# Kernel tuning notes

Measured on AMD Instinct MI355X. Metric: run time of the kernel, lower is better.

The kernel has to match this reference:

```python
import jax, jax.numpy as jnp
import numpy as np

B, T, D, H = 4, 2048, 1024, 16
DK = D // H


def setup_inputs() -> dict:
    key = jax.random.key(0)
    ks = jax.random.split(key, 9)
    s = 1.0 / np.sqrt(D)
    x = jax.random.normal(ks[0], (B, T, D), dtype=jnp.float32)
    mask = jnp.tril(jnp.ones((T, T), dtype=bool))[None, None]  # causal [1,1,T,T]
    wq = jax.random.uniform(ks[1], (D, D), jnp.float32, -s, s)
    bq = jax.random.uniform(ks[2], (D,), jnp.float32, -s, s)
    wk = jax.random.uniform(ks[3], (D, D), jnp.float32, -s, s)
    bk = jax.random.uniform(ks[4], (D,), jnp.float32, -s, s)
    wv = jax.random.uniform(ks[5], (D, D), jnp.float32, -s, s)
    bv = jax.random.uniform(ks[6], (D,), jnp.float32, -s, s)
    wo = jax.random.uniform(ks[7], (D, D), jnp.float32, -s, s)
    bo = jax.random.uniform(ks[8], (D,), jnp.float32, -s, s)
    return {"x": x, "mask": mask, "wq": wq, "bq": bq, "wk": wk, "bk": bk,
            "wv": wv, "bv": bv, "wo": wo, "bo": bo}


def reference(x, mask, wq, bq, wk, bk, wv, bv, wo, bo):
    # projections: torch Linear is x @ W.T + b; here weights stored as (D, D) used directly
    q = (x @ wq + bq).reshape(B, T, H, DK).transpose(0, 2, 1, 3)  # [B,H,T,dk]
    k = (x @ wk + bk).reshape(B, T, H, DK).transpose(0, 2, 1, 3)
    v = (x @ wv + bv).reshape(B, T, H, DK).transpose(0, 2, 1, 3)
    scores = jnp.einsum('bhqd,bhkd->bhqk', q, k) / jnp.sqrt(jnp.float32(DK))
    scores = jnp.where(mask, scores, -jnp.inf)
    attn = jax.nn.softmax(scores, axis=-1)
    # dropout p=0.0 -> identity
    y = jnp.einsum('bhqk,bhkd->bhqd', attn, v)
    y = y.transpose(0, 2, 1, 3).reshape(B, T, D)
    return y @ wo + bo
```

## Files before the change

### kernel.cpp

```cpp
#include <hip/hip_runtime.h>


typedef short s16x8 __attribute__((ext_vector_type(8)));
typedef short s16x4 __attribute__((ext_vector_type(4)));
typedef float f32x4 __attribute__((ext_vector_type(4)));
typedef unsigned int u32x2 __attribute__((ext_vector_type(2)));
typedef unsigned short u16x4 __attribute__((ext_vector_type(4)));

static __device__ __forceinline__ float bf2f(unsigned short u) {
    return __uint_as_float(((unsigned int)u) << 16);
}
static __device__ __forceinline__ unsigned short f2bf(float f) {
    unsigned int x = __float_as_uint(f);
    unsigned int r = x + 0x7fffu + ((x >> 16) & 1u);
    return (unsigned short)(r >> 16);
}

static __device__ __forceinline__ void gload_lds16(const short* g, short* l) {
    __builtin_amdgcn_global_load_lds((__attribute__((address_space(1))) void*)g,
                                     (__attribute__((address_space(3))) void*)l, 16, 0, 0);
}

static __device__ __forceinline__ unsigned int cvt_pk_bf16(float a, float b) {
    unsigned int r;
    asm("v_cvt_pk_bf16_f32 %0, %1, %2" : "=v"(r) : "v"(a), "v"(b));
    return r;
}

static __device__ __forceinline__ float fexp2(float x) {
    float r;
    asm("v_exp_f32 %0, %1" : "=v"(r) : "v"(x));
    return r;
}

__global__ __launch_bounds__(64) void detect_dtype(const unsigned short* __restrict__ x,
                                                   int* __restrict__ flag) {
    int lane = threadIdx.x;
    int cnt = 0;
    for (int i = 0; i < 64; ++i) {
        float v = bf2f(x[lane * 64 + i]);
        if (!(fabsf(v) < 1e10f)) cnt++;
    }
    unsigned long long m = __ballot(cnt > 0);
    if (lane == 0) *flag = (m != 0ull) ? 1 : 0;
}

__global__ __launch_bounds__(256) void prep(const void* __restrict__ x,
                                            const void* __restrict__ b0, const void* __restrict__ b1,
                                            const void* __restrict__ b2, const void* __restrict__ b3,
                                            const void* __restrict__ w0, const void* __restrict__ w1,
                                            const void* __restrict__ w2, const void* __restrict__ w3,
                                            unsigned short* __restrict__ xb,
                                            unsigned short* __restrict__ bb,
                                            unsigned short* __restrict__ wT,
                                            const int* __restrict__ flag) {
    __shared__ unsigned short t[32][33];
    int bid = blockIdx.x, tid = threadIdx.x;
    int f = *flag;
    if (bid < 8192) {
        int i = bid * 256 + tid;
        u16x4 o;
        if (f) {
            float4 v = ((const float4*)x)[i];
            o[0] = f2bf(v.x); o[1] = f2bf(v.y); o[2] = f2bf(v.z); o[3] = f2bf(v.w);
        } else {
            o = ((const u16x4*)x)[i];
        }
        ((u16x4*)xb)[i] = o;
    } else if (bid < 8208) {
        int i = (bid - 8192) * 256 + tid;
        const void* src = (i < 1024) ? b0 : (i < 2048 ? b1 : (i < 3072 ? b2 : b3));
        int k = i & 1023;
        bb[i] = f ? f2bf(((const float*)src)[k]) : ((const unsigned short*)src)[k];
    } else {
        int tz = bid - 8208;
        int z = tz >> 10, tile = tz & 1023;
        const void* src = (z == 0) ? w0 : (z == 1 ? w1 : (z == 2 ? w2 : w3));
        unsigned short* dst = wT + (size_t)z * 1024 * 1024;
        int xx = tid & 31, yy = tid >> 5;
        int n0 = (tile & 31) * 32, k0 = (tile >> 5) * 32;
        for (int j = 0; j < 32; j += 8) {
            size_t idx = (size_t)(k0 + yy + j) * 1024 + n0 + xx;
            t[yy + j][xx] = f ? f2bf(((const float*)src)[idx]) : ((const unsigned short*)src)[idx];
        }
        __syncthreads();
        for (int j = 0; j < 32; j += 8) dst[(size_t)(n0 + yy + j) * 1024 + k0 + xx] = t[xx][yy + j];
    }
}

__global__ __launch_bounds__(256) void gemm_bf16(const short* __restrict__ A,
                                                 const short* __restrict__ Bt,
                                                 void* __restrict__ C,
                                                 short* __restrict__ vt,
                                                 const unsigned short* __restrict__ bq,
                                                 const unsigned short* __restrict__ bk,
                                                 const unsigned short* __restrict__ bv,
                                                 int K, int ldc,
                                                 const int* __restrict__ flag, int f32out,
                                                 int scale_q, int fuse_v) {
    __shared__ __align__(16) short As[2][128][64];
    __shared__ __align__(16) short Bs[2][128][64];
    int tid = threadIdx.x;
    int wid = tid >> 6, lane = tid & 63, quad = lane >> 4, l16 = lane & 15;
    int wm = wid & 1, wn = wid >> 1;
    int m0 = blockIdx.x * 128, n0 = blockIdx.y * 128;
    bool wf = f32out && (*flag != 0);

    int srow = lane >> 3;
    int schunk = (lane & 7) ^ srow;
    const short* Ag = A  + (size_t)(m0 + wid * 32 + srow) * K + schunk * 8;
    const short* Bg = Bt + (size_t)(n0 + wid * 32 + srow) * K + schunk * 8;

    f32x4 acc[4][4] = {};
    int nt = K >> 6;

#pragma unroll
    for (int c = 0; c < 4; ++c) {
        gload_lds16(Ag + c * 8 * K, &As[0][wid * 32 + c * 8][0]);
        gload_lds16(Bg + c * 8 * K, &Bs[0][wid * 32 + c * 8][0]);
    }
    __syncthreads();

    for (int t = 0; t < nt; ++t) {
        if (t + 1 < nt) {
            int bu = (t + 1) & 1;
            int kof = (t + 1) * 64;
#pragma unroll
            for (int c = 0; c < 4; ++c) {
                gload_lds16(Ag + kof + c * 8 * K, &As[bu][wid * 32 + c * 8][0]);
                gload_lds16(Bg + kof + c * 8 * K, &Bs[bu][wid * 32 + c * 8][0]);
            }
        }
        const short (*Ab)[64] = As[t & 1];
#pragma unroll
        for (int kk = 0; kk < 2; ++kk) {
            s16x8 a[4], b[4];
#pragma unroll
            for (int i = 0; i < 4; ++i) {
                int row = wm * 64 + i * 16 + l16;
                a[i] = *(const s16x8*)&Ab[row][(((kk << 2) + quad) ^ (row & 7)) << 3];
            }
#pragma unroll
            for (int j = 0; j < 4; ++j) {
                int row = wn * 64 + j * 16 + l16;
                b[j] = *(const s16x8*)&Bs[t & 1][row][(((kk << 2) + quad) ^ (row & 7)) << 3];
            }
            __builtin_amdgcn_s_setprio(1);
#pragma unroll
            for (int i = 0; i < 4; ++i)
#pragma unroll
                for (int j = 0; j < 4; ++j)
                    acc[i][j] = __builtin_amdgcn_mfma_f32_16x16x32_bf16(a[i], b[j], acc[i][j], 0, 0, 0);
            __builtin_amdgcn_s_setprio(0);
        }
        __syncthreads();
    }
    for (int j = 0; j < 4; ++j) {
        int col = n0 + wn * 64 + j * 16 + l16;
        const unsigned short* bptr = (col < 1024) ? bq : (col < 2048 ? bk : bv);
        float bias = bf2f(bptr[col & 1023]);
        float cs = (scale_q && col < 1024) ? 0.18033688f : 1.0f;
        for (int i = 0; i < 4; ++i) {
            int rbase = m0 + wm * 64 + i * 16 + quad * 4;
            if (fuse_v && col >= 2048) {
                int h = (col - 2048) >> 6, dk = col & 63;
                int bb_ = rbase >> 11, t = rbase & 2047;
                s16x4 pk;
                for (int r = 0; r < 4; ++r) pk[r] = (short)f2bf(acc[i][j][r] + bias);
                *(s16x4*)(vt + ((size_t)((bb_ * 16 + h) * 64 + dk)) * 2048 + t) = pk;
            } else {
                for (int r = 0; r < 4; ++r) {
                    float v = (acc[i][j][r] + bias) * cs;
                    size_t idx = (size_t)(rbase + r) * ldc + col;
                    if (wf) ((float*)C)[idx] = v;
                    else    ((unsigned short*)C)[idx] = f2bf(v);
                }
            }
        }
    }
}

static __device__ __forceinline__ void stage_tiles(const short* kbase, const short* vbase,
                                                   int kt, short* Kb, short* Vb,
                                                   int wid, int lane) {
    int row = wid * 8 + (lane >> 3);
    int c_src = (lane & 7) ^ (lane >> 3);
    const short* kg = kbase + (size_t)(kt * 64 + row) * 3072 + c_src * 8;
    const short* vg = vbase + (size_t)row * 2048 + kt * 64 + c_src * 8;
    gload_lds16(kg, Kb + wid * 512);
    gload_lds16(vg, Vb + wid * 512);
}

static __device__ __forceinline__ s16x8 lds_frag(const short* buf, int row, int cg) {
    int slot = cg ^ (row & 7);
    return *(const s16x8*)(buf + row * 64 + slot * 8);
}

__global__ __launch_bounds__(512, 4) void attn(const short* __restrict__ qkv,
                                               const short* __restrict__ vt,
                                               unsigned short* __restrict__ y) {
    __shared__ __align__(16) short Kbuf[3][64 * 64];
    __shared__ __align__(16) short Vbuf[3][64 * 64];
    __shared__ __align__(16) short Ps[8][16 * 68];
    int tid = threadIdx.x;
    int wid = tid >> 6, lane = tid & 63, quad = lane >> 4, l16 = lane & 15;
    int bh = blockIdx.x, b = bh >> 4, h = bh & 15;
    const short* kbase = qkv + (size_t)b * 2048 * 3072 + 1024 + h * 64;
    const short* vbase = vt + (size_t)bh * 64 * 2048;
    short* PsW = &Ps[wid][0];

    s16x8 ones;
    for (int e = 0; e < 8; ++e) ones[e] = (short)0x3F80;

    int qb = 15 - (int)blockIdx.y;
    int ktmax = 2 * qb + 1;
    int kmax_w = 2 * qb + (wid >> 2);

    const short* qp = qkv + (size_t)(b * 2048 + qb * 128 + wid * 16 + l16) * 3072 + h * 64;
    s16x8 q0 = *(const s16x8*)(qp + quad * 8);
    s16x8 q1 = *(const s16x8*)(qp + 32 + quad * 8);

    float m_old = -INFINITY;
    f32x4 lacc = {0.f, 0.f, 0.f, 0.f};
    f32x4 o[4] = {};
    s16x8 paA, paB;
    s16x8 vr[8];
    bool have_prev = false;

    stage_tiles(kbase, vbase, 0, &Kbuf[0][0], &Vbuf[0][0], wid, lane);
    stage_tiles(kbase, vbase, 1, &Kbuf[1][0], &Vbuf[1][0], wid, lane);
    int ss = 2;
    int cc = 0;

    for (int kt = 0; kt <= ktmax; ++kt) {
        if (kt < ktmax) asm volatile("s_waitcnt vmcnt(2)" ::: "memory");
        else            asm volatile("s_waitcnt vmcnt(0)" ::: "memory");
        __builtin_amdgcn_sched_barrier(0);
        __builtin_amdgcn_s_barrier();

        if (kt + 2 <= ktmax) {
            stage_tiles(kbase, vbase, kt + 2, &Kbuf[0][0] + ss * 4096, &Vbuf[0][0] + ss * 4096,
                        wid, lane);
            ss = (ss == 2) ? 0 : ss + 1;
        }

        if (kt <= kmax_w) {
            const short* Kb = &Kbuf[0][0] + cc * 4096;
            const short* Vb = &Vbuf[0][0] + cc * 4096;

            f32x4 s[4] = {};
            __builtin_amdgcn_s_setprio(1);
            for (int j = 0; j < 4; ++j) {
                s16x8 klo = lds_frag(Kb, j * 16 + l16, quad);
                s16x8 khi = lds_frag(Kb, j * 16 + l16, 4 + quad);
                s[j] = __builtin_amdgcn_mfma_f32_16x16x32_bf16(klo, q0, s[j], 0, 0, 0);
                s[j] = __builtin_amdgcn_mfma_f32_16x16x32_bf16(khi, q1, s[j], 0, 0, 0);
            }
            if (have_prev) {
                lacc = __builtin_amdgcn_mfma_f32_16x16x32_bf16(paA, ones, lacc, 0, 0, 0);
                lacc = __builtin_amdgcn_mfma_f32_16x16x32_bf16(paB, ones, lacc, 0, 0, 0);
                for (int d = 0; d < 4; ++d) {
                    o[d] = __builtin_amdgcn_mfma_f32_16x16x32_bf16(paA, vr[2 * d], o[d], 0, 0, 0);
                    o[d] = __builtin_amdgcn_mfma_f32_16x16x32_bf16(paB, vr[2 * d + 1], o[d], 0, 0, 0);
                }
            }
            __builtin_amdgcn_s_setprio(0);

            if (kt == kmax_w) {
                int qq = (wid & 3) * 16 + l16;
                for (int j = 0; j < 4; ++j)
                    for (int r = 0; r < 4; ++r)
                        if (j * 16 + quad * 4 + r > qq) s[j][r] = -INFINITY;
            }

            float mj0 = fmaxf(fmaxf(s[0][0], s[0][1]), s[0][2]);
            mj0 = fmaxf(mj0, s[0][3]);
            float mj1 = fmaxf(fmaxf(s[1][0], s[1][1]), s[1][2]);
            mj1 = fmaxf(mj1, s[1][3]);
            float mj2 = fmaxf(fmaxf(s[2][0], s[2][1]), s[2][2]);
            mj2 = fmaxf(mj2, s[2][3]);
            float mj3 = fmaxf(fmaxf(s[3][0], s[3][1]), s[3][2]);
            mj3 = fmaxf(mj3, s[3][3]);
            float mx = fmaxf(fmaxf(fmaxf(mj0, mj1), mj2), mj3);
            mx = fmaxf(mx, __shfl_xor(mx, 16));
            mx = fmaxf(mx, __shfl_xor(mx, 32));

            if (__any(mx > m_old + 8.0f)) {
                float mn = fmaxf(m_old, mx);
                float alpha = fexp2(m_old - mn);
                m_old = mn;
                float ar[4];
                for (int r = 0; r < 4; ++r) ar[r] = __shfl(alpha, quad * 4 + r);
                for (int r = 0; r < 4; ++r) {
                    lacc[r] *= ar[r];
                    for (int d = 0; d < 4; ++d) o[d][r] *= ar[r];
                }
            }

            for (int j = 0; j < 4; ++j) {
                float p0 = fexp2(s[j][0] - m_old);
                float p1 = fexp2(s[j][1] - m_old);
                float p2 = fexp2(s[j][2] - m_old);
                float p3 = fexp2(s[j][3] - m_old);
                u32x2 w;
                w.x = cvt_pk_bf16(p0, p1);
                w.y = cvt_pk_bf16(p2, p3);
                *(u32x2*)(PsW + l16 * 68 + j * 16 + quad * 4) = w;
            }
            paA = *(const s16x8*)&PsW[l16 * 68 + quad * 8];
            paB = *(const s16x8*)&PsW[l16 * 68 + 32 + quad * 8];

            for (int d = 0; d < 4; ++d) {
                vr[2 * d]     = lds_frag(Vb, d * 16 + l16, quad);
                vr[2 * d + 1] = lds_frag(Vb, d * 16 + l16, 4 + quad);
            }
            have_prev = true;
        }
        cc = (cc == 2) ? 0 : cc + 1;
    }

    if (have_prev) {
        __builtin_amdgcn_s_setprio(1);
        lacc = __builtin_amdgcn_mfma_f32_16x16x32_bf16(paA, ones, lacc, 0, 0, 0);
        lacc = __builtin_amdgcn_mfma_f32_16x16x32_bf16(paB, ones, lacc, 0, 0, 0);
        for (int d = 0; d < 4; ++d) {
            o[d] = __builtin_amdgcn_mfma_f32_16x16x32_bf16(paA, vr[2 * d], o[d], 0, 0, 0);
            o[d] = __builtin_amdgcn_mfma_f32_16x16x32_bf16(paB, vr[2 * d + 1], o[d], 0, 0, 0);
        }
        __builtin_amdgcn_s_setprio(0);
    }

    for (int r = 0; r < 4; ++r) {
        float inv = 1.f / lacc[r];
        int t = qb * 128 + wid * 16 + quad * 4 + r;
        for (int d = 0; d < 4; ++d)
            y[(size_t)(b * 2048 + t) * 1024 + h * 64 + d * 16 + l16] = f2bf(o[d][r] * inv);
    }
}

extern "C" void kernel_launch(void* const* d_in, const int* in_sizes, int n_in,
                              void* d_out, int out_size, void* d_ws, size_t ws_size,
                              hipStream_t stream) {
    (void)in_sizes; (void)n_in; (void)out_size; (void)ws_size;
    const void* x  = d_in[0];
    const void* wq = d_in[2]; const void* bq = d_in[3];
    const void* wk = d_in[4]; const void* bk = d_in[5];
    const void* wv = d_in[6]; const void* bv = d_in[7];
    const void* wo = d_in[8]; const void* bo = d_in[9];

    const size_t MB = 1024 * 1024;
    char* ws = (char*)d_ws;
    unsigned short* wT  = (unsigned short*)ws;
    short* qkv = (short*)(ws + 8 * MB);
    short* vt  = (short*)(ws + 56 * MB);
    unsigned short* xb = (unsigned short*)(ws + 72 * MB);
    unsigned short* yb = (unsigned short*)(ws + 72 * MB);
    unsigned short* bb = (unsigned short*)(ws + 88 * MB);
    int* flag = (int*)(ws + 88 * MB + 64 * 1024);

    detect_dtype<<<1, 64, 0, stream>>>((const unsigned short*)x, flag);
    prep<<<12304, 256, 0, stream>>>(x, bq, bk, bv, bo, wq, wk, wv, wo, xb, bb, wT, flag);

    gemm_bf16<<<dim3(64, 24), 256, 0, stream>>>((const short*)xb, (const short*)wT,
                                                qkv, vt, bb, bb + 1024, bb + 2048,
                                                1024, 3072, flag, 0, 1, 1);
    attn<<<dim3(64, 16), 512, 0, stream>>>(qkv, vt, yb);
    gemm_bf16<<<dim3(64, 8), 256, 0, stream>>>((const short*)yb, (const short*)(wT + 3072 * 1024),
                                               d_out, nullptr, bb + 3072, bb + 3072, bb + 3072,
                                               1024, 1024, flag, 1, 0, 0);
}
```

Measured before the change: 292.1 us.

## Add 256x256-tile QKV GEMM and un-pipeline PV MMAs in attention

Replaces the 128x128 QKV projection GEMM with a new 512-thread kernel using 256x256 tiles, XOR-swizzled LDS and direct global-to-LDS loads. The larger tile raises arithmetic intensity per LDS byte, at the cost of fewer blocks (384) and heavy register use per thread. The attention kernel also drops its software pipelining of the P·V and row-sum MFMAs into the next iteration and now issues them right after the softmax of the same tile. This cuts the registers held across iterations but exposes the latency between the exp step and the MFMAs.

```diff
diff --git a/kernel.cpp b/kernel.cpp
--- a/kernel.cpp
+++ b/kernel.cpp
@@ -88,6 +88,96 @@
     }
 }
 
+__global__ __launch_bounds__(512, 1) void gemm256(const short* __restrict__ A,
+                                                  const short* __restrict__ Bt,
+                                                  unsigned short* __restrict__ qkv,
+                                                  short* __restrict__ vt,
+                                                  const unsigned short* __restrict__ bq,
+                                                  const unsigned short* __restrict__ bk,
+                                                  const unsigned short* __restrict__ bv) {
+    const int K = 1024;
+    __shared__ __align__(16) short As[2][256][64];
+    __shared__ __align__(16) short Bs[2][256][64];
+    int tid = threadIdx.x;
+    int wid = tid >> 6, lane = tid & 63, quad = lane >> 4, l16 = lane & 15;
+    int wm = wid >> 2;
+    int wn = wid & 3;
+    int m0 = blockIdx.x * 256, n0 = blockIdx.y * 256;
+
+    int srow = lane >> 3;
+    int schunk = (lane & 7) ^ srow;
+    const short* Ag = A  + (size_t)(m0 + wid * 32 + srow) * K + schunk * 8;
+    const short* Bg = Bt + (size_t)(n0 + wid * 32 + srow) * K + schunk * 8;
+
+    f32x4 acc[8][4] = {};
+    const int nt = K >> 6;
+
+#pragma unroll
+    for (int c = 0; c < 4; ++c) {
+        gload_lds16(Ag + c * 8 * K, &As[0][wid * 32 + c * 8][0]);
+        gload_lds16(Bg + c * 8 * K, &Bs[0][wid * 32 + c * 8][0]);
+    }
+    __syncthreads();
+
+    for (int t = 0; t < nt; ++t) {
+        if (t + 1 < nt) {
+            int bu = (t + 1) & 1;
+            int kof = (t + 1) * 64;
+#pragma unroll
+            for (int c = 0; c < 4; ++c) {
+                gload_lds16(Ag + kof + c * 8 * K, &As[bu][wid * 32 + c * 8][0]);
+                gload_lds16(Bg + kof + c * 8 * K, &Bs[bu][wid * 32 + c * 8][0]);
+            }
+        }
+#pragma unroll
+        for (int kk = 0; kk < 2; ++kk) {
+            s16x8 a[8], b[4];
+#pragma unroll
+            for (int i = 0; i < 8; ++i) {
+                int row = wm * 128 + i * 16 + l16;
+                a[i] = *(const s16x8*)&As[t & 1][row][(((kk << 2) + quad) ^ (row & 7)) << 3];
+            }
+#pragma unroll
+            for (int j = 0; j < 4; ++j) {
+                int row = wn * 64 + j * 16 + l16;
+                b[j] = *(const s16x8*)&Bs[t & 1][row][(((kk << 2) + quad) ^ (row & 7)) << 3];
+            }
+            __builtin_amdgcn_s_setprio(1);
+#pragma unroll
+            for (int i = 0; i < 8; ++i)
+#pragma unroll
+                for (int j = 0; j < 4; ++j)
+                    acc[i][j] = __builtin_amdgcn_mfma_f32_16x16x32_bf16(a[i], b[j], acc[i][j], 0, 0, 0);
+            __builtin_amdgcn_s_setprio(0);
+        }
+        __syncthreads();
+    }
+
+#pragma unroll
+    for (int j = 0; j < 4; ++j) {
+        int col = n0 + wn * 64 + j * 16 + l16;
+        const unsigned short* bptr = (col < 1024) ? bq : (col < 2048 ? bk : bv);
+        float bias = bf2f(bptr[col & 1023]);
+        float cs = (col < 1024) ? 0.18033688f : 1.0f;
+#pragma unroll
+        for (int i = 0; i < 8; ++i) {
+            int rbase = m0 + wm * 128 + i * 16 + quad * 4;
+            if (col >= 2048) {
+                int h = (col - 2048) >> 6, dk = col & 63;
+                int bb_ = rbase >> 11, tt = rbase & 2047;
+                s16x4 pk;
+                for (int r = 0; r < 4; ++r) pk[r] = (short)f2bf(acc[i][j][r] + bias);
+                *(s16x4*)(vt + ((size_t)((bb_ * 16 + h) * 64 + dk)) * 2048 + tt) = pk;
+            } else {
+                for (int r = 0; r < 4; ++r) {
+                    float v = (acc[i][j][r] + bias) * cs;
+                    qkv[(size_t)(rbase + r) * 3072 + col] = f2bf(v);
+                }
+            }
+        }
+    }
+}
+
 __global__ __launch_bounds__(256) void gemm_bf16(const short* __restrict__ A,
                                                  const short* __restrict__ Bt,
                                                  void* __restrict__ C,
@@ -223,9 +313,6 @@
     float m_old = -INFINITY;
     f32x4 lacc = {0.f, 0.f, 0.f, 0.f};
     f32x4 o[4] = {};
-    s16x8 paA, paB;
-    s16x8 vr[8];
-    bool have_prev = false;
 
     stage_tiles(kbase, vbase, 0, &Kbuf[0][0], &Vbuf[0][0], wid, lane);
     stage_tiles(kbase, vbase, 1, &Kbuf[1][0], &Vbuf[1][0], wid, lane);
@@ -255,14 +342,6 @@
                 s16x8 khi = lds_frag(Kb, j * 16 + l16, 4 + quad);
                 s[j] = __builtin_amdgcn_mfma_f32_16x16x32_bf16(klo, q0, s[j], 0, 0, 0);
                 s[j] = __builtin_amdgcn_mfma_f32_16x16x32_bf16(khi, q1, s[j], 0, 0, 0);
-            }
-            if (have_prev) {
-                lacc = __builtin_amdgcn_mfma_f32_16x16x32_bf16(paA, ones, lacc, 0, 0, 0);
-                lacc = __builtin_amdgcn_mfma_f32_16x16x32_bf16(paB, ones, lacc, 0, 0, 0);
-                for (int d = 0; d < 4; ++d) {
-                    o[d] = __builtin_amdgcn_mfma_f32_16x16x32_bf16(paA, vr[2 * d], o[d], 0, 0, 0);
-                    o[d] = __builtin_amdgcn_mfma_f32_16x16x32_bf16(paB, vr[2 * d + 1], o[d], 0, 0, 0);
-                }
             }
             __builtin_amdgcn_s_setprio(0);
 
@@ -307,27 +386,21 @@
                 w.y = cvt_pk_bf16(p2, p3);
                 *(u32x2*)(PsW + l16 * 68 + j * 16 + quad * 4) = w;
             }
-            paA = *(const s16x8*)&PsW[l16 * 68 + quad * 8];
-            paB = *(const s16x8*)&PsW[l16 * 68 + 32 + quad * 8];
-
+
+            s16x8 pa0 = *(const s16x8*)&PsW[l16 * 68 + quad * 8];
+            s16x8 pa1 = *(const s16x8*)&PsW[l16 * 68 + 32 + quad * 8];
+            __builtin_amdgcn_s_setprio(1);
+            lacc = __builtin_amdgcn_mfma_f32_16x16x32_bf16(pa0, ones, lacc, 0, 0, 0);
+            lacc = __builtin_amdgcn_mfma_f32_16x16x32_bf16(pa1, ones, lacc, 0, 0, 0);
             for (int d = 0; d < 4; ++d) {
-                vr[2 * d]     = lds_frag(Vb, d * 16 + l16, quad);
-                vr[2 * d + 1] = lds_frag(Vb, d * 16 + l16, 4 + quad);
-            }
-            have_prev = true;
+                s16x8 vlo = lds_frag(Vb, d * 16 + l16, quad);
+                s16x8 vhi = lds_frag(Vb, d * 16 + l16, 4 + quad);
+                o[d] = __builtin_amdgcn_mfma_f32_16x16x32_bf16(pa0, vlo, o[d], 0, 0, 0);
+                o[d] = __builtin_amdgcn_mfma_f32_16x16x32_bf16(pa1, vhi, o[d], 0, 0, 0);
+            }
+            __builtin_amdgcn_s_setprio(0);
         }
         cc = (cc == 2) ? 0 : cc + 1;
-    }
-
-    if (have_prev) {
-        __builtin_amdgcn_s_setprio(1);
-        lacc = __builtin_amdgcn_mfma_f32_16x16x32_bf16(paA, ones, lacc, 0, 0, 0);
-        lacc = __builtin_amdgcn_mfma_f32_16x16x32_bf16(paB, ones, lacc, 0, 0, 0);
-        for (int d = 0; d < 4; ++d) {
-            o[d] = __builtin_amdgcn_mfma_f32_16x16x32_bf16(paA, vr[2 * d], o[d], 0, 0, 0);
-            o[d] = __builtin_amdgcn_mfma_f32_16x16x32_bf16(paB, vr[2 * d + 1], o[d], 0, 0, 0);
-        }
-        __builtin_amdgcn_s_setprio(0);
     }
 
     for (int r = 0; r < 4; ++r) {
@@ -361,9 +434,9 @@
     detect_dtype<<<1, 64, 0, stream>>>((const unsigned short*)x, flag);
     prep<<<12304, 256, 0, stream>>>(x, bq, bk, bv, bo, wq, wk, wv, wo, xb, bb, wT, flag);
 
-    gemm_bf16<<<dim3(64, 24), 256, 0, stream>>>((const short*)xb, (const short*)wT,
-                                                qkv, vt, bb, bb + 1024, bb + 2048,
-                                                1024, 3072, flag, 0, 1, 1);
+    gemm256<<<dim3(32, 12), 512, 0, stream>>>((const short*)xb, (const short*)wT,
+                                              (unsigned short*)qkv, vt,
+                                              bb, bb + 1024, bb + 2048);
     attn<<<dim3(64, 16), 512, 0, stream>>>(qkv, vt, yb);
     gemm_bf16<<<dim3(64, 8), 256, 0, stream>>>((const short*)yb, (const short*)(wT + 3072 * 1024),
                                                d_out, nullptr, bb + 3072, bb + 3072, bb + 3072,
```

Measured after the change: 303.9 us. 1.04x slower.

## Fold dtype detection into prep kernel and de-pipeline attention PV step

Applied to the files above, without the earlier changes.

Removes the separate single-block dtype-detection launch by having every prep block recompute the flag from the first 4096 input elements, with block 0 writing it to global memory for the later GEMMs. In the attention kernel, the software pipelining that deferred the P·V and row-sum MFMAs to the next iteration is dropped: P·V now runs right after the softmax in the same iteration, with V fragments loaded from LDS inline. This saves a kernel launch and frees the registers that held the carried P and V fragments. The cost is that every prep block rereads the input sample, and the attention loop loses the overlap between QK^T and the previous tile's PV MFMAs.

```diff
diff --git a/kernel.cpp b/kernel.cpp
--- a/kernel.cpp
+++ b/kernel.cpp
@@ -31,18 +31,6 @@
     float r;
     asm("v_exp_f32 %0, %1" : "=v"(r) : "v"(x));
     return r;
-}
-
-__global__ __launch_bounds__(64) void detect_dtype(const unsigned short* __restrict__ x,
-                                                   int* __restrict__ flag) {
-    int lane = threadIdx.x;
-    int cnt = 0;
-    for (int i = 0; i < 64; ++i) {
-        float v = bf2f(x[lane * 64 + i]);
-        if (!(fabsf(v) < 1e10f)) cnt++;
-    }
-    unsigned long long m = __ballot(cnt > 0);
-    if (lane == 0) *flag = (m != 0ull) ? 1 : 0;
 }
 
 __global__ __launch_bounds__(256) void prep(const void* __restrict__ x,
@@ -53,10 +41,27 @@
                                             unsigned short* __restrict__ xb,
                                             unsigned short* __restrict__ bb,
                                             unsigned short* __restrict__ wT,
-                                            const int* __restrict__ flag) {
+                                            int* __restrict__ flag) {
     __shared__ unsigned short t[32][33];
+    __shared__ int sflag;
     int bid = blockIdx.x, tid = threadIdx.x;
-    int f = *flag;
+
+    {
+        const unsigned short* xs = (const unsigned short*)x;
+        bool big = false;
+        for (int k = 0; k < 16; ++k) {
+            float v = bf2f(xs[tid * 16 + k]);
+            big |= !(fabsf(v) < 1e10f);
+        }
+        unsigned long long m = __ballot(big);
+        if (tid == 0) sflag = 0;
+        __syncthreads();
+        if ((tid & 63) == 0 && m != 0ull) sflag = 1;
+        __syncthreads();
+    }
+    int f = sflag;
+    if (bid == 0 && tid == 0) *flag = f;
+
     if (bid < 8192) {
         int i = bid * 256 + tid;
         u16x4 o;
@@ -223,9 +228,6 @@
     float m_old = -INFINITY;
     f32x4 lacc = {0.f, 0.f, 0.f, 0.f};
     f32x4 o[4] = {};
-    s16x8 paA, paB;
-    s16x8 vr[8];
-    bool have_prev = false;
 
     stage_tiles(kbase, vbase, 0, &Kbuf[0][0], &Vbuf[0][0], wid, lane);
     stage_tiles(kbase, vbase, 1, &Kbuf[1][0], &Vbuf[1][0], wid, lane);
@@ -255,14 +257,6 @@
                 s16x8 khi = lds_frag(Kb, j * 16 + l16, 4 + quad);
                 s[j] = __builtin_amdgcn_mfma_f32_16x16x32_bf16(klo, q0, s[j], 0, 0, 0);
                 s[j] = __builtin_amdgcn_mfma_f32_16x16x32_bf16(khi, q1, s[j], 0, 0, 0);
-            }
-            if (have_prev) {
-                lacc = __builtin_amdgcn_mfma_f32_16x16x32_bf16(paA, ones, lacc, 0, 0, 0);
-                lacc = __builtin_amdgcn_mfma_f32_16x16x32_bf16(paB, ones, lacc, 0, 0, 0);
-                for (int d = 0; d < 4; ++d) {
-                    o[d] = __builtin_amdgcn_mfma_f32_16x16x32_bf16(paA, vr[2 * d], o[d], 0, 0, 0);
-                    o[d] = __builtin_amdgcn_mfma_f32_16x16x32_bf16(paB, vr[2 * d + 1], o[d], 0, 0, 0);
-                }
             }
             __builtin_amdgcn_s_setprio(0);
 
@@ -307,27 +301,21 @@
                 w.y = cvt_pk_bf16(p2, p3);
                 *(u32x2*)(PsW + l16 * 68 + j * 16 + quad * 4) = w;
             }
-            paA = *(const s16x8*)&PsW[l16 * 68 + quad * 8];
-            paB = *(const s16x8*)&PsW[l16 * 68 + 32 + quad * 8];
-
+
+            s16x8 pa0 = *(const s16x8*)&PsW[l16 * 68 + quad * 8];
+            s16x8 pa1 = *(const s16x8*)&PsW[l16 * 68 + 32 + quad * 8];
+            __builtin_amdgcn_s_setprio(1);
+            lacc = __builtin_amdgcn_mfma_f32_16x16x32_bf16(pa0, ones, lacc, 0, 0, 0);
+            lacc = __builtin_amdgcn_mfma_f32_16x16x32_bf16(pa1, ones, lacc, 0, 0, 0);
             for (int d = 0; d < 4; ++d) {
-                vr[2 * d]     = lds_frag(Vb, d * 16 + l16, quad);
-                vr[2 * d + 1] = lds_frag(Vb, d * 16 + l16, 4 + quad);
-            }
-            have_prev = true;
+                s16x8 vlo = lds_frag(Vb, d * 16 + l16, quad);
+                s16x8 vhi = lds_frag(Vb, d * 16 + l16, 4 + quad);
+                o[d] = __builtin_amdgcn_mfma_f32_16x16x32_bf16(pa0, vlo, o[d], 0, 0, 0);
+                o[d] = __builtin_amdgcn_mfma_f32_16x16x32_bf16(pa1, vhi, o[d], 0, 0, 0);
+            }
+            __builtin_amdgcn_s_setprio(0);
         }
         cc = (cc == 2) ? 0 : cc + 1;
-    }
-
-    if (have_prev) {
-        __builtin_amdgcn_s_setprio(1);
-        lacc = __builtin_amdgcn_mfma_f32_16x16x32_bf16(paA, ones, lacc, 0, 0, 0);
-        lacc = __builtin_amdgcn_mfma_f32_16x16x32_bf16(paB, ones, lacc, 0, 0, 0);
-        for (int d = 0; d < 4; ++d) {
-            o[d] = __builtin_amdgcn_mfma_f32_16x16x32_bf16(paA, vr[2 * d], o[d], 0, 0, 0);
-            o[d] = __builtin_amdgcn_mfma_f32_16x16x32_bf16(paB, vr[2 * d + 1], o[d], 0, 0, 0);
-        }
-        __builtin_amdgcn_s_setprio(0);
     }
 
     for (int r = 0; r < 4; ++r) {
@@ -358,7 +346,6 @@
     unsigned short* bb = (unsigned short*)(ws + 88 * MB);
     int* flag = (int*)(ws + 88 * MB + 64 * 1024);
 
-    detect_dtype<<<1, 64, 0, stream>>>((const unsigned short*)x, flag);
     prep<<<12304, 256, 0, stream>>>(x, bq, bk, bv, bo, wq, wk, wv, wo, xb, bb, wT, flag);
 
     gemm_bf16<<<dim3(64, 24), 256, 0, stream>>>((const short*)xb, (const short*)wT,
```

Measured after the change: 291.0 us. Within noise of the previous version (-0.4%).
